# Kernel tuning notes

Measured on AMD Instinct MI355X. Metric: run time of the kernel, lower is better.

Reference implementation:

```python
import jax, jax.numpy as jnp
import numpy as np

B, T, C, H = 16, 512, 256, 8
HS_T = C // H   # temporal head size = 32
HS_S = T // H   # spatial head size = 64
EPS = 1e-6


def _ln(x, w, b):
    m = x.mean(-1, keepdims=True)
    v = ((x - m) ** 2).mean(-1, keepdims=True)
    return (x - m) / jnp.sqrt(v + EPS) * w + b


def setup_inputs() -> dict:
    key = jax.random.key(0)
    ks = jax.random.split(key, 16)
    rn = lambda k, s, scale: jax.random.normal(k, s, dtype=jnp.float32) * scale
    inp = {
        "x_T": rn(ks[0], (B, T, C), 1.0),
        "x_S": rn(ks[1], (B, C, T), 1.0),
        # temporal attention: per-head q/k/v projections, stacked [H, hs, C]
        "Wq_t": rn(ks[2], (H, HS_T, C), C ** -0.5),
        "Wk_t": rn(ks[3], (H, HS_T, C), C ** -0.5),
        "Wv_t": rn(ks[4], (H, HS_T, C), C ** -0.5),
        "Wo": rn(ks[5], (C, C), C ** -0.5),
        # spatial attention: per-head q/k over the time axis, stacked [H, hs_s, T]
        "Wq_s": rn(ks[6], (H, HS_S, T), T ** -0.5),
        "Wk_s": rn(ks[7], (H, HS_S, T), T ** -0.5),
        # feed-forward blocks (expansion_factor=4)
        "ff1_w1": rn(ks[8], (4 * C, C), C ** -0.5),
        "ff1_b1": jnp.zeros((4 * C,), jnp.float32),
        "ff1_w2": rn(ks[9], (C, 4 * C), (4 * C) ** -0.5),
        "ff1_b2": jnp.zeros((C,), jnp.float32),
        "ff2_w1": rn(ks[10], (4 * C, C), C ** -0.5),
        "ff2_b1": jnp.zeros((4 * C,), jnp.float32),
        "ff2_w2": rn(ks[11], (C, 4 * C), (4 * C) ** -0.5),
        "ff2_b2": jnp.zeros((C,), jnp.float32),
        # layernorm affine params
        "t_ln1_w": jnp.ones((C,), jnp.float32), "t_ln1_b": jnp.zeros((C,), jnp.float32),
        "t_ln2_w": jnp.ones((C,), jnp.float32), "t_ln2_b": jnp.zeros((C,), jnp.float32),
        "s_ln1_w": jnp.ones((T,), jnp.float32), "s_ln1_b": jnp.zeros((T,), jnp.float32),
        "fus_ln_w": jnp.ones((C,), jnp.float32), "fus_ln_b": jnp.zeros((C,), jnp.float32),
    }
    return inp


def reference(x_T, x_S, Wq_t, Wk_t, Wv_t, Wo, Wq_s, Wk_s,
              ff1_w1, ff1_b1, ff1_w2, ff1_b2, ff2_w1, ff2_b1, ff2_w2, ff2_b2,
              t_ln1_w, t_ln1_b, t_ln2_w, t_ln2_b, s_ln1_w, s_ln1_b,
              fus_ln_w, fus_ln_b):
    # ---- temporal (causal) multi-head attention ----
    h = _ln(x_T, t_ln1_w, t_ln1_b)                         # [B,T,C]
    q = jnp.einsum('btc,hdc->bhtd', h, Wq_t)
    k = jnp.einsum('btc,hdc->bhtd', h, Wk_t)
    v = jnp.einsum('btc,hdc->bhtd', h, Wv_t)
    scores = jnp.einsum('bhtd,bhsd->bhts', q, k) / jnp.sqrt(jnp.float32(HS_T))
    causal = jnp.tril(jnp.ones((T, T), dtype=bool))
    scores = jnp.where(causal, scores, -jnp.inf)
    att = jax.nn.softmax(scores, axis=-1)
    o = jnp.einsum('bhts,bhsd->bhtd', att, v)              # [B,H,T,hs]
    o = o.transpose(0, 2, 1, 3).reshape(B, T, C)           # concat heads
    attn_out = o @ Wo.T
    x = x_T + attn_out
    # FFN 1
    h2 = _ln(x, t_ln2_w, t_ln2_b)
    f = jax.nn.relu(h2 @ ff1_w1.T + ff1_b1) @ ff1_w2.T + ff1_b2
    temporal_out = x + f                                   # [B,T,C]
    # ---- spatial (non-causal) attention over neurons ----
    hs = _ln(x_S, s_ln1_w, s_ln1_b)                        # [B,C,T]
    qs = jnp.einsum('bct,hdt->bhcd', hs, Wq_s)
    ks = jnp.einsum('bct,hdt->bhcd', hs, Wk_s)
    sc = jnp.einsum('bhcd,bhed->bhce', qs, ks) / jnp.sqrt(jnp.float32(HS_S))
    spatial_weights = jax.nn.softmax(sc, axis=-1).mean(axis=1)   # [B,C,C], mean over heads
    # ---- fusion ----
    fused = jnp.einsum('bce,bte->btc', spatial_weights, temporal_out)
    x2 = temporal_out + fused
    h3 = _ln(x2, fus_ln_w, fus_ln_b)
    f2 = jax.nn.relu(h3 @ ff2_w1.T + ff2_b1) @ ff2_w2.T + ff2_b2
    out = x2 + f2
    return out, spatial_weights
```

## Files before the change

kernel.cpp:

```cpp
#include <hip/hip_runtime.h>
#include <hip/hip_bf16.h>

typedef __hip_bfloat16 bf16;
typedef __attribute__((ext_vector_type(8))) short short8;
typedef __attribute__((ext_vector_type(4))) float f32x4;

#define F_BIAS 1
#define F_RELU 2
#define F_RES  4

__device__ __forceinline__ void st_out(float* p, float v){ *p = v; }
__device__ __forceinline__ void st_out(bf16* p, float v){ *p = __float2bfloat16(v); }
__device__ __forceinline__ short f2bs(float f){
  bf16 h = __float2bfloat16(f);
  return *reinterpret_cast<short*>(&h);
}

__device__ __forceinline__ void gl_lds16(const void* g, void* l){
  __builtin_amdgcn_global_load_lds(
      (const __attribute__((address_space(1))) void*)g,
      (__attribute__((address_space(3))) void*)l, 16, 0, 0);
}

__device__ __forceinline__ void lgkm_barrier(){
  asm volatile("s_waitcnt lgkmcnt(0)" ::: "memory");
  __builtin_amdgcn_s_barrier();
}

struct ProArgs {
  const float* wsrc[10];
  bf16* wdst[10];
  const float *xT, *xS, *tl1w, *tl1b, *sl1w, *sl1b;
  bf16 *hT, *hS;
};

template<int RL>
__device__ __forceinline__ void wave_ln(bf16* __restrict__ dst,
    const float* __restrict__ src, const float* __restrict__ w,
    const float* __restrict__ bvec, int row){
  int lane = threadIdx.x & 63;
  const float* s = src + (size_t)row*RL;
  float4 v0 = *(const float4*)(s + lane*4);
  float4 v1 = {0.f,0.f,0.f,0.f};
  float sum = v0.x+v0.y+v0.z+v0.w;
  float sq  = v0.x*v0.x+v0.y*v0.y+v0.z*v0.z+v0.w*v0.w;
  if (RL == 512){
    v1 = *(const float4*)(s + 256 + lane*4);
    sum += v1.x+v1.y+v1.z+v1.w;
    sq  += v1.x*v1.x+v1.y*v1.y+v1.z*v1.z+v1.w*v1.w;
  }
  #pragma unroll
  for (int off=32; off; off>>=1){
    sum += __shfl_xor(sum, off, 64);
    sq  += __shfl_xor(sq , off, 64);
  }
  const float inv = 1.0f/(float)RL;
  float mean = sum*inv;
  float rstd = rsqrtf(sq*inv - mean*mean + 1e-6f);
  float4 w0 = *(const float4*)(w + lane*4);
  float4 b0 = *(const float4*)(bvec + lane*4);
  bf16* d = dst + (size_t)row*RL;
  short4 o;
  o.x = f2bs((v0.x-mean)*rstd*w0.x + b0.x);
  o.y = f2bs((v0.y-mean)*rstd*w0.y + b0.y);
  o.z = f2bs((v0.z-mean)*rstd*w0.z + b0.z);
  o.w = f2bs((v0.w-mean)*rstd*w0.w + b0.w);
  *(short4*)((short*)d + lane*4) = o;
  if (RL == 512){
    float4 w1 = *(const float4*)(w + 256 + lane*4);
    float4 b1 = *(const float4*)(bvec + 256 + lane*4);
    short4 o1;
    o1.x = f2bs((v1.x-mean)*rstd*w1.x + b1.x);
    o1.y = f2bs((v1.y-mean)*rstd*w1.y + b1.y);
    o1.z = f2bs((v1.z-mean)*rstd*w1.z + b1.z);
    o1.w = f2bs((v1.w-mean)*rstd*w1.w + b1.w);
    *(short4*)((short*)d + 256 + lane*4) = o1;
  }
}

__global__ __launch_bounds__(256) void prologue(ProArgs a){
  int blk = blockIdx.x;
  int wid = threadIdx.x >> 6;
  if (blk < 1792){
    int v = blk*256 + threadIdx.x;
    int e = v*4;
    int seg = (e>=65536)+(e>=131072)+(e>=196608)+(e>=262144)+(e>=524288)
            + (e>=786432)+(e>=1048576)+(e>=1310720)+(e>=1572864);
    const int starts[10] = {0,65536,131072,196608,262144,524288,786432,
                            1048576,1310720,1572864};
    int off = e - starts[seg];
    float4 f = *(const float4*)(a.wsrc[seg] + off);
    short4 o;
    o.x = f2bs(f.x); o.y = f2bs(f.y); o.z = f2bs(f.z); o.w = f2bs(f.w);
    *(short4*)((short*)a.wdst[seg] + off) = o;
  } else if (blk < 1792 + 2048){
    wave_ln<256>(a.hT, a.xT, a.tl1w, a.tl1b, (blk-1792)*4 + wid);
  } else {
    wave_ln<512>(a.hS, a.xS, a.sl1w, a.sl1b, (blk-3840)*4 + wid);
  }
}

template<int BM, int BN, int BK>
__device__ __forceinline__ void gemm_body(
    short* __restrict__ AsB, short* __restrict__ BsB,
    const bf16* __restrict__ A, const bf16* __restrict__ B,
    float* __restrict__ outF, bf16* __restrict__ outB,
    const float* __restrict__ bias, const float* __restrict__ resid,
    int K, int lda, int ldb, int ldc, int flags, int m0, int n0){
  int tid = threadIdx.x;
  int w = tid>>6, lane = tid&63, quad = lane>>4, l16 = lane&15;
  constexpr int MF  = BM/32;
  constexpr int NF  = BN/32;
  constexpr int CPR = BK/8;
  constexpr int CA  = BM*CPR/256;
  constexpr int CB  = BN*CPR/256;
  int wm = (w>>1)*(BM/2), wn = (w&1)*(BN/2);
  f32x4 acc[MF][NF];
  #pragma unroll
  for (int r=0;r<MF;r++)
    #pragma unroll
    for (int j=0;j<NF;j++)
      acc[r][j] = (f32x4){0.f,0.f,0.f,0.f};

  auto stage = [&](int k0, int half){
    short* as = AsB + half*(BM*BK);
    short* bs = BsB + half*(BN*BK);
    #pragma unroll
    for (int c=0;c<CA;c++){
      int ch = tid + c*256;
      int row = ch / CPR, p = ch % CPR;
      gl_lds16(A + (size_t)(m0+row)*lda + k0 + ((p ^ (row&(CPR-1)))*8),
               &as[row*BK + p*8]);
    }
    #pragma unroll
    for (int c=0;c<CB;c++){
      int ch = tid + c*256;
      int row = ch / CPR, p = ch % CPR;
      gl_lds16(B + (size_t)(n0+row)*ldb + k0 + ((p ^ (row&(CPR-1)))*8),
               &bs[row*BK + p*8]);
    }
  };

  stage(0, 0);
  int nk = K / BK;
  for (int t = 0; t < nk; ++t){
    __syncthreads();
    if (t+1 < nk) stage((t+1)*BK, (t+1)&1);
    const short* as = AsB + (t&1)*(BM*BK);
    const short* bs = BsB + (t&1)*(BN*BK);
    #pragma unroll
    for (int ks=0; ks<BK/32; ++ks){
      short8 af[MF], bfr[NF];
      #pragma unroll
      for (int r=0;r<MF;r++){
        int rr = wm + r*16 + l16;
        af[r] = *(short8*)&as[rr*BK + (((ks*4+quad) ^ (rr&(CPR-1)))*8)];
      }
      #pragma unroll
      for (int j=0;j<NF;j++){
        int rr = wn + j*16 + l16;
        bfr[j] = *(short8*)&bs[rr*BK + (((ks*4+quad) ^ (rr&(CPR-1)))*8)];
      }
      #pragma unroll
      for (int r=0;r<MF;r++)
        #pragma unroll
        for (int j=0;j<NF;j++)
          acc[r][j] = __builtin_amdgcn_mfma_f32_16x16x32_bf16(af[r], bfr[j], acc[r][j], 0,0,0);
    }
  }
  #pragma unroll
  for (int r=0;r<MF;r++){
    int mb = m0 + wm + r*16 + quad*4;
    #pragma unroll
    for (int j=0;j<NF;j++){
      int n = n0 + wn + j*16 + l16;
      float bv = (flags & F_BIAS) ? bias[n] : 0.0f;
      #pragma unroll
      for (int e=0;e<4;e++){
        float v = acc[r][j][e] + bv;
        if (flags & F_RELU) v = fmaxf(v, 0.0f);
        long long idx = (long long)(mb+e)*ldc + n;
        if (flags & F_RES) v += resid[idx];
        if (outF) outF[idx] = v;
        if (outB) st_out(outB + idx, v);
      }
    }
  }
}

struct GArgs {
  const bf16 *A, *B;
  float* outF; bf16* outB;
  const float *bias, *resid;
  int K, lda, ldb, ldc, flags, ty;
};
__global__ __launch_bounds__(256) void gemm_dual(GArgs g0, GArgs g1, int n0){
  __shared__ __align__(16) short As[2*64*64];
  __shared__ __align__(16) short Bs[2*128*64];
  int id = blockIdx.x;
  bool first = id < n0;
  const GArgs& g = first ? g0 : g1;
  int t = first ? id : id - n0;
  int bx = t / g.ty, by = t - bx*g.ty;
  gemm_body<64,128,64>(As, Bs, g.A, g.B, g.outF, g.outB, g.bias, g.resid,
                       g.K, g.lda, g.ldb, g.ldc, g.flags, bx*64, by*128);
}

__global__ __launch_bounds__(512) void gemm_ln(
    const bf16* __restrict__ A, const bf16* __restrict__ B,
    float* __restrict__ outF, bf16* __restrict__ outLN,
    const float* __restrict__ resid,
    const float* __restrict__ lnw, const float* __restrict__ lnb,
    int K, int lda, int ldb, int flags,
    long long sA, long long sB, long long sO, long long sR){
  int bz = blockIdx.z;
  A += (size_t)bz*sA;
  B += (size_t)bz*sB;
  long long obase = (long long)bz*sO;
  __shared__ __align__(16) short As[2*32*64];
  __shared__ __align__(16) short Bs[2*256*64];
  __shared__ float redS[4][32], redQ[4][32];
  int tid = threadIdx.x;
  int m0 = blockIdx.x*32;
  int w = tid>>6, lane = tid&63, quad = lane>>4, l16 = lane&15;
  int wm = (w>>2)*16;
  int wn = (w&3)*64;
  f32x4 acc[4];
  #pragma unroll
  for (int j=0;j<4;j++) acc[j] = (f32x4){0.f,0.f,0.f,0.f};

  auto stage = [&](int k0, int half){
    short* as = As + half*(32*64);
    short* bs = Bs + half*(256*64);
    if (tid < 256){
      int row = tid >> 3, p = tid & 7;
      gl_lds16(A + (size_t)(m0+row)*lda + k0 + ((p ^ (row&7))*8),
               &as[row*64 + p*8]);
    }
    #pragma unroll
    for (int c=0;c<4;c++){
      int ch = tid + c*512;
      int row = ch >> 3, p = ch & 7;
      gl_lds16(B + (size_t)row*ldb + k0 + ((p ^ (row&7))*8),
               &bs[row*64 + p*8]);
    }
  };

  stage(0, 0);
  int nk = K / 64;
  for (int t = 0; t < nk; ++t){
    __syncthreads();
    if (t+1 < nk) stage((t+1)*64, (t+1)&1);
    const short* as = As + (t&1)*(32*64);
    const short* bs = Bs + (t&1)*(256*64);
    #pragma unroll
    for (int ks=0; ks<2; ++ks){
      int rr = wm + l16;
      short8 af = *(short8*)&as[rr*64 + (((ks*4+quad) ^ (rr&7))*8)];
      #pragma unroll
      for (int j=0;j<4;j++){
        int rb = wn + j*16 + l16;
        short8 bfr = *(short8*)&bs[rb*64 + (((ks*4+quad) ^ (rb&7))*8)];
        acc[j] = __builtin_amdgcn_mfma_f32_16x16x32_bf16(af, bfr, acc[j], 0,0,0);
      }
    }
  }
  #pragma unroll
  for (int e=0;e<4;e++){
    int row = wm + quad*4 + e;
    float s = 0.f, q2 = 0.f;
    #pragma unroll
    for (int j=0;j<4;j++){
      float v = acc[j][e];
      if (flags & F_RES)
        v += resid[(long long)bz*sR + (long long)(m0+row)*256 + wn + j*16 + l16];
      acc[j][e] = v;
      s += v; q2 += v*v;
    }
    #pragma unroll
    for (int off=1; off<16; off<<=1){
      s  += __shfl_xor(s , off, 16);
      q2 += __shfl_xor(q2, off, 16);
    }
    if (l16==0){ redS[w&3][row] = s; redQ[w&3][row] = q2; }
  }
  __syncthreads();
  #pragma unroll
  for (int e=0;e<4;e++){
    int row = wm + quad*4 + e;
    float tot = redS[0][row] + redS[1][row] + redS[2][row] + redS[3][row];
    float tq  = redQ[0][row] + redQ[1][row] + redQ[2][row] + redQ[3][row];
    float mean = tot * (1.0f/256.0f);
    float var  = tq * (1.0f/256.0f) - mean*mean;
    float rstd = rsqrtf(var + 1e-6f);
    #pragma unroll
    for (int j=0;j<4;j++){
      int col = wn + j*16 + l16;
      float v = acc[j][e];
      long long idx = obase + (long long)(m0+row)*256 + col;
      if (outF) outF[idx] = v;
      outLN[idx] = __float2bfloat16((v-mean)*rstd*lnw[col] + lnb[col]);
    }
  }
}

struct FfnArgs {
  const bf16 *A;
  const bf16 *W1;
  const float *B1;
  const bf16 *W2;
  const float *B2;
  const float *resid;
  float *outF;
  bf16  *outB;
};

__global__ __launch_bounds__(512) void ffn(FfnArgs a){
  __shared__ __align__(16) short Afull[32*256];
  __shared__ __align__(16) short Hs[32*1024];
  __shared__ __align__(16) short Bst[2*16384];
  int tid = threadIdx.x;
  int w = tid>>6, lane = tid&63, quad = lane>>4, l16 = lane&15;
  int m0 = blockIdx.x*32;
  int wm  = (w>>2)*16;
  int wnA = (w&3)*32;
  int wnB = (w&3)*64;

  #pragma unroll
  for (int c=0;c<2;c++){
    int ch = tid + c*512;
    int row = ch>>5, p = ch&31;
    gl_lds16(a.A + (size_t)(m0+row)*256 + ((p ^ row)*8), &Afull[ch*8]);
  }
  auto stageA = [&](int i, int half){
    short* bs = Bst + half*16384;
    int nc = i>>2, kt = i&3;
    #pragma unroll
    for (int c=0;c<2;c++){
      int ch = tid + c*512;
      int row = ch>>3, p = ch&7;
      gl_lds16(a.W1 + (size_t)(nc*128+row)*256 + kt*64 + ((p ^ (row&7))*8),
               &bs[ch*8]);
    }
  };
  auto stageB = [&](int kt, int half){
    short* bs = Bst + half*16384;
    #pragma unroll
    for (int c=0;c<4;c++){
      int ch = tid + c*512;
      int row = ch>>3, p = ch&7;
      gl_lds16(a.W2 + (size_t)row*1024 + kt*64 + ((p ^ (row&7))*8),
               &bs[ch*8]);
    }
  };

  stageA(0, 0);
  f32x4 acc[2];
  for (int i=0; i<32; ++i){
    __syncthreads();
    if (i+1 < 32) stageA(i+1, (i+1)&1);
    const short* bs = Bst + (i&1)*16384;
    int kt = i&3, nc = i>>2;
    if (kt==0){
      acc[0] = (f32x4){0.f,0.f,0.f,0.f};
      acc[1] = (f32x4){0.f,0.f,0.f,0.f};
    }
    #pragma unroll
    for (int ks=0; ks<2; ++ks){
      int rr = wm + l16;
      int kk = kt*8 + ks*4 + quad;
      short8 af = *(short8*)&Afull[rr*256 + ((kk ^ rr)*8)];
      #pragma unroll
      for (int j=0;j<2;j++){
        int rb = wnA + j*16 + l16;
        short8 bk = *(short8*)&bs[rb*64 + (((ks*4+quad) ^ (rb&7))*8)];
        acc[j] = __builtin_amdgcn_mfma_f32_16x16x32_bf16(af, bk, acc[j], 0,0,0);
      }
    }
    if (kt==3){
      #pragma unroll
      for (int j=0;j<2;j++)
        #pragma unroll
        for (int e=0;e<4;e++){
          int row = wm + quad*4 + e;
          int col = nc*128 + wnA + j*16 + l16;
          float v = fmaxf(acc[j][e] + a.B1[col], 0.0f);
          int grp = col>>3;
          Hs[row*1024 + ((grp ^ (row&7))<<3) + (col&7)] = f2bs(v);
        }
    }
  }

  stageB(0, 0);
  __syncthreads();
  f32x4 accB[4];
  #pragma unroll
  for (int j=0;j<4;j++) accB[j] = (f32x4){0.f,0.f,0.f,0.f};
  for (int kt=0; kt<16; ++kt){
    if (kt) __syncthreads();
    if (kt+1 < 16) stageB(kt+1, (kt+1)&1);
    const short* bs = Bst + (kt&1)*16384;
    #pragma unroll
    for (int ks=0; ks<2; ++ks){
      int rr = wm + l16;
      int kk = kt*8 + ks*4 + quad;
      short8 af = *(short8*)&Hs[rr*1024 + ((kk ^ (rr&7))*8)];
      #pragma unroll
      for (int j=0;j<4;j++){
        int rb = wnB + j*16 + l16;
        short8 bk = *(short8*)&bs[rb*64 + (((ks*4+quad) ^ (rb&7))*8)];
        accB[j] = __builtin_amdgcn_mfma_f32_16x16x32_bf16(af, bk, accB[j], 0,0,0);
      }
    }
  }
  #pragma unroll
  for (int j=0;j<4;j++){
    int n = wnB + j*16 + l16;
    float bv = a.B2[n];
    #pragma unroll
    for (int e=0;e<4;e++){
      int row = m0 + wm + quad*4 + e;
      long long idx = (long long)row*256 + n;
      float v = accB[j][e] + bv + a.resid[idx];
      a.outF[idx] = v;
      if (a.outB) st_out(a.outB + idx, v);
    }
  }
}

__device__ __forceinline__ int fsw(int row){ return (row>>1)&3; }
__global__ __launch_bounds__(256) void flash_mfma(
    const bf16* __restrict__ qkv, bf16* __restrict__ o){
  int qt = (int)gridDim.x - 1 - (int)blockIdx.x;
  int h = blockIdx.y, b = blockIdx.z;
  int tid = threadIdx.x;
  int w = tid>>6, lane = tid&63, quad = lane>>4, l16 = lane&15;
  __shared__ __align__(16) bf16 Qs[64*32];
  __shared__ __align__(16) bf16 Ks[2][64*32];
  __shared__ __align__(16) bf16 Vt[2][32*72];
  __shared__ __align__(16) bf16 Ps[64*72];
  const bf16* base = qkv + (size_t)b*512*768;
  int t0 = qt*64;
  int srow = tid>>2, spos = tid&3;
  gl_lds16(base + (size_t)(t0+srow)*768 + h*32 + ((spos ^ fsw(srow))*8),
           &Qs[srow*32 + spos*8]);
  {
    const bf16* rp = base + (size_t)srow*768 + h*32;
    gl_lds16(rp + 256 + ((spos ^ fsw(srow))*8), &Ks[0][srow*32 + spos*8]);
    short8 v = *(const short8*)(rp + 512 + spos*8);
    #pragma unroll
    for (int q=0;q<8;q++){
      short tmp = v[q];
      Vt[0][(spos*8+q)*72 + srow] = *(bf16*)&tmp;
    }
  }
  f32x4 accO[2];
  accO[0] = (f32x4){0.f,0.f,0.f,0.f};
  accO[1] = (f32x4){0.f,0.f,0.f,0.f};
  float m_i[4], l_i[4];
  #pragma unroll
  for (int e=0;e<4;e++){ m_i[e] = -3.0e38f; l_i[e] = 0.0f; }
  const float scale = 0.17677669529663687f;
  __syncthreads();
  int rq = w*16 + l16;
  short8 aq = *(short8*)&Qs[rq*32 + ((quad ^ fsw(rq))*8)];

  for (int kt = 0; kt <= qt; ++kt){
    if (kt) __syncthreads();
    int cur = kt&1, nxt = cur^1;
    bool pre = (kt < qt);
    short8 vpre;
    if (pre){
      const bf16* rp = base + (size_t)((kt+1)*64 + srow)*768 + h*32;
      gl_lds16(rp + 256 + ((spos ^ fsw(srow))*8), &Ks[nxt][srow*32 + spos*8]);
      vpre = *(const short8*)(rp + 512 + spos*8);
    }
    f32x4 S[4];
    #pragma unroll
    for (int j2=0;j2<4;j2++){
      int rk = j2*16 + l16;
      short8 bk = *(short8*)&Ks[cur][rk*32 + ((quad ^ fsw(rk))*8)];
      S[j2] = __builtin_amdgcn_mfma_f32_16x16x32_bf16(aq, bk,
                (f32x4){0.f,0.f,0.f,0.f}, 0,0,0);
    }
    bool diag = (kt == qt);
    int s0 = kt*64;
    int qrow_base = t0 + w*16 + quad*4;
    #pragma unroll
    for (int e=0;e<4;e++){
      float sv[4];
      #pragma unroll
      for (int j2=0;j2<4;j2++){
        float x = S[j2][e]*scale;
        if (diag && (s0 + j2*16 + l16 > qrow_base + e)) x = -3.0e38f;
        sv[j2] = x;
      }
      float mx = fmaxf(fmaxf(sv[0],sv[1]), fmaxf(sv[2],sv[3]));
      #pragma unroll
      for (int off=1; off<16; off<<=1) mx = fmaxf(mx, __shfl_xor(mx, off, 64));
      float m_new = fmaxf(m_i[e], mx);
      float alpha = __expf(m_i[e]-m_new);
      float rs = 0.0f;
      #pragma unroll
      for (int j2=0;j2<4;j2++){
        float p = __expf(sv[j2]-m_new);
        rs += p;
        Ps[(w*16+quad*4+e)*72 + j2*16 + l16] = __float2bfloat16(p);
      }
      #pragma unroll
      for (int off=1; off<16; off<<=1) rs += __shfl_xor(rs, off, 64);
      l_i[e] = l_i[e]*alpha + rs;
      m_i[e] = m_new;
      accO[0][e] *= alpha;
      accO[1][e] *= alpha;
    }
    asm volatile("s_waitcnt lgkmcnt(0)" ::: "memory");
    __builtin_amdgcn_sched_barrier(0);
    #pragma unroll
    for (int sh=0; sh<2; ++sh){
      short8 ap = *(short8*)&Ps[(w*16+l16)*72 + sh*32 + quad*8];
      #pragma unroll
      for (int dh=0; dh<2; ++dh){
        short8 bv = *(short8*)&Vt[cur][(dh*16+l16)*72 + sh*32 + quad*8];
        accO[dh] = __builtin_amdgcn_mfma_f32_16x16x32_bf16(ap, bv, accO[dh], 0,0,0);
      }
    }
    if (pre){
      #pragma unroll
      for (int q=0;q<8;q++){
        short tmp = vpre[q];
        Vt[nxt][(spos*8+q)*72 + srow] = *(bf16*)&tmp;
      }
    }
  }
  #pragma unroll
  for (int e=0;e<4;e++){
    float inv = 1.0f/l_i[e];
    int t = t0 + w*16 + quad*4 + e;
    bf16* op = o + ((size_t)(b*512+t))*256 + h*32 + l16;
    op[0]  = __float2bfloat16(accO[0][e]*inv);
    op[16] = __float2bfloat16(accO[1][e]*inv);
  }
}

__global__ __launch_bounds__(256) void spatial_fused(
    const bf16* __restrict__ qk, float* __restrict__ out1,
    bf16* __restrict__ swB){
  int ct = blockIdx.x & 15, b = blockIdx.x >> 4;
  int tid = threadIdx.x;
  int w = tid>>6, lane = tid&63, quad = lane>>4, l16 = lane&15;
  __shared__ __align__(16) bf16 Qall[16*512];
  __shared__ __align__(16) bf16 Ks[2][256*64];
  __shared__ float redM[4][16], redS2[4][16];
  const bf16* qbase = qk + ((size_t)(b*256 + ct*16))*1024;
  #pragma unroll
  for (int c=0;c<4;c++){
    int ch = tid + c*256;
    int row = ch>>6, p = ch&63;
    gl_lds16(qbase + (size_t)row*1024 + ((p ^ (row&7))*8), &Qall[row*512 + p*8]);
  }
  auto stageK = [&](int h, int half){
    bf16* ks = Ks[half];
    #pragma unroll
    for (int c=0;c<8;c++){
      int ch = tid + c*256;
      int e = ch>>3, p = ch&7;
      gl_lds16(qk + ((size_t)(b*256 + e))*1024 + 512 + h*64 + ((p ^ (e&7))*8),
               &ks[e*64 + p*8]);
    }
  };
  stageK(0, 0);
  float fRes[4][4];
  #pragma unroll
  for (int j=0;j<4;j++)
    #pragma unroll
    for (int e=0;e<4;e++) fRes[j][e] = 0.0f;

  for (int h=0; h<8; ++h){
    __syncthreads();
    if (h+1 < 8) stageK(h+1, (h+1)&1);
    const bf16* kcur = Ks[h&1];
    f32x4 acc[4];
    #pragma unroll
    for (int j=0;j<4;j++) acc[j] = (f32x4){0.f,0.f,0.f,0.f};
    #pragma unroll
    for (int ki=0; ki<2; ++ki){
      int g = h*8 + ki*4 + quad;
      short8 aq = *(short8*)&Qall[l16*512 + ((g ^ (l16&7))*8)];
      #pragma unroll
      for (int j=0;j<4;j++){
        int e = w*64 + j*16 + l16;
        short8 bk = *(short8*)&kcur[e*64 + (((ki*4+quad) ^ (e&7))*8)];
        acc[j] = __builtin_amdgcn_mfma_f32_16x16x32_bf16(aq, bk, acc[j], 0,0,0);
      }
    }
    #pragma unroll
    for (int e=0;e<4;e++){
      float m = -3.0e38f;
      #pragma unroll
      for (int j=0;j<4;j++){
        float s = acc[j][e]*0.125f;
        acc[j][e] = s;
        m = fmaxf(m, s);
      }
      #pragma unroll
      for (int off=1; off<16; off<<=1) m = fmaxf(m, __shfl_xor(m, off, 16));
      if (l16==0) redM[w][quad*4+e] = m;
    }
    lgkm_barrier();
    #pragma unroll
    for (int e=0;e<4;e++){
      int r = quad*4+e;
      float m = fmaxf(fmaxf(redM[0][r],redM[1][r]), fmaxf(redM[2][r],redM[3][r]));
      float s = 0.0f;
      #pragma unroll
      for (int j=0;j<4;j++){
        float p = __expf(acc[j][e]-m);
        acc[j][e] = p; s += p;
      }
      #pragma unroll
      for (int off=1; off<16; off<<=1) s += __shfl_xor(s, off, 16);
      if (l16==0) redS2[w][r] = s;
    }
    lgkm_barrier();
    #pragma unroll
    for (int e=0;e<4;e++){
      int r = quad*4+e;
      float tot = redS2[0][r]+redS2[1][r]+redS2[2][r]+redS2[3][r];
      float inv = 0.125f/tot;
      #pragma unroll
      for (int j=0;j<4;j++) fRes[j][e] += acc[j][e]*inv;
    }
  }
  #pragma unroll
  for (int e=0;e<4;e++){
    int c = ct*16 + quad*4 + e;
    size_t rb = ((size_t)b*256 + c)*256;
    #pragma unroll
    for (int j=0;j<4;j++){
      int col = w*64 + j*16 + l16;
      out1[rb+col] = fRes[j][e];
      swB[rb+col]  = __float2bfloat16(fRes[j][e]);
    }
  }
}

extern "C" void kernel_launch(void* const* d_in, const int* in_sizes, int n_in,
                              void* d_out, int out_size, void* d_ws, size_t ws_size,
                              hipStream_t stream){
  (void)in_sizes; (void)n_in; (void)out_size; (void)ws_size;
  const float* x_T  = (const float*)d_in[0];
  const float* x_S  = (const float*)d_in[1];
  const float* Wq_t = (const float*)d_in[2];
  const float* Wk_t = (const float*)d_in[3];
  const float* Wv_t = (const float*)d_in[4];
  const float* Wo   = (const float*)d_in[5];
  const float* Wq_s = (const float*)d_in[6];
  const float* Wk_s = (const float*)d_in[7];
  const float* f1w1 = (const float*)d_in[8];
  const float* f1b1 = (const float*)d_in[9];
  const float* f1w2 = (const float*)d_in[10];
  const float* f1b2 = (const float*)d_in[11];
  const float* f2w1 = (const float*)d_in[12];
  const float* f2b1 = (const float*)d_in[13];
  const float* f2w2 = (const float*)d_in[14];
  const float* f2b2 = (const float*)d_in[15];
  const float* tl1w = (const float*)d_in[16];
  const float* tl1b = (const float*)d_in[17];
  const float* tl2w = (const float*)d_in[18];
  const float* tl2b = (const float*)d_in[19];
  const float* sl1w = (const float*)d_in[20];
  const float* sl1b = (const float*)d_in[21];
  const float* flw  = (const float*)d_in[22];
  const float* flb  = (const float*)d_in[23];

  float* ws = (float*)d_ws;
  size_t off = 0;
  bf16*  Wqkvb  = (bf16*)(ws + off); off += 768*256/2;
  bf16*  Wob    = (bf16*)(ws + off); off += 256*256/2;
  bf16*  f1w1b  = (bf16*)(ws + off); off += 1024*256/2;
  bf16*  f1w2b  = (bf16*)(ws + off); off += 256*1024/2;
  bf16*  f2w1b  = (bf16*)(ws + off); off += 1024*256/2;
  bf16*  f2w2b  = (bf16*)(ws + off); off += 256*1024/2;
  bf16*  WSb    = (bf16*)(ws + off); off += 1024*512/2;
  bf16*  bufHb  = (bf16*)(ws + off); off += (size_t)8192*256/2;
  bf16*  bufHSb = (bf16*)(ws + off); off += (size_t)4096*512/2;
  bf16*  bufQKVb= (bf16*)(ws + off); off += (size_t)8192*768/2;
  bf16*  bufOb  = (bf16*)(ws + off); off += (size_t)8192*256/2;
  bf16*  bufTOb = (bf16*)(ws + off); off += (size_t)8192*256/2;
  bf16*  swB    = (bf16*)(ws + off); off += (size_t)16*256*256/2;
  bf16*  qkB    = (bf16*)(ws + off); off += (size_t)4096*1024/2;
  float* bufX   = ws + off; off += (size_t)8192*256;
  float* bufTO  = ws + off; off += (size_t)8192*256;
  float* bufX2  = ws + off; off += (size_t)8192*256;

  float* out0 = (float*)d_out;
  float* out1 = out0 + (size_t)16*512*256;

  ProArgs pa;
  pa.wsrc[0]=Wq_t;  pa.wdst[0]=Wqkvb;
  pa.wsrc[1]=Wk_t;  pa.wdst[1]=Wqkvb+65536;
  pa.wsrc[2]=Wv_t;  pa.wdst[2]=Wqkvb+131072;
  pa.wsrc[3]=Wo;    pa.wdst[3]=Wob;
  pa.wsrc[4]=f1w1;  pa.wdst[4]=f1w1b;
  pa.wsrc[5]=f1w2;  pa.wdst[5]=f1w2b;
  pa.wsrc[6]=f2w1;  pa.wdst[6]=f2w1b;
  pa.wsrc[7]=f2w2;  pa.wdst[7]=f2w2b;
  pa.wsrc[8]=Wq_s;  pa.wdst[8]=WSb;
  pa.wsrc[9]=Wk_s;  pa.wdst[9]=WSb+262144;
  pa.xT=x_T; pa.xS=x_S; pa.tl1w=tl1w; pa.tl1b=tl1b;
  pa.sl1w=sl1w; pa.sl1b=sl1b; pa.hT=bufHb; pa.hS=bufHSb;
  prologue<<<4864,256,0,stream>>>(pa);

  GArgs gq, gs;
  gq.A=bufHb;  gq.B=Wqkvb; gq.outF=nullptr; gq.outB=bufQKVb;
  gq.bias=nullptr; gq.resid=nullptr;
  gq.K=256; gq.lda=256; gq.ldb=256; gq.ldc=768; gq.flags=0; gq.ty=6;
  gs.A=bufHSb; gs.B=WSb;   gs.outF=nullptr; gs.outB=qkB;
  gs.bias=nullptr; gs.resid=nullptr;
  gs.K=512; gs.lda=512; gs.ldb=512; gs.ldc=1024; gs.flags=0; gs.ty=8;
  gemm_dual<<<1280,256,0,stream>>>(gq, gs, 768);

  spatial_fused<<<256,256,0,stream>>>(qkB, out1, swB);

  flash_mfma<<<dim3(8,8,16),256,0,stream>>>(bufQKVb, bufOb);
  gemm_ln<<<dim3(256,1,1),512,0,stream>>>(bufOb, Wob, bufX, bufHb,
        x_T, tl2w, tl2b, 256, 256,256, F_RES, 0,0,0,0);
  FfnArgs fa1;
  fa1.A=bufHb; fa1.W1=f1w1b; fa1.B1=f1b1; fa1.W2=f1w2b; fa1.B2=f1b2;
  fa1.resid=bufX; fa1.outF=bufTO; fa1.outB=bufTOb;
  ffn<<<256,512,0,stream>>>(fa1);
  gemm_ln<<<dim3(16,1,16),512,0,stream>>>(bufTOb, swB, bufX2, bufHb,
        bufTO, flw, flb, 256, 256,256, F_RES,
        131072, 65536, 131072, 131072);
  FfnArgs fa2;
  fa2.A=bufHb; fa2.W1=f2w1b; fa2.B1=f2b1; fa2.W2=f2w2b; fa2.B2=f2b2;
  fa2.resid=bufX2; fa2.outF=out0; fa2.outB=nullptr;
  ffn<<<256,512,0,stream>>>(fa2);
}
```

Measured before the change: 294.2 us.

## Fuse GEMM+LayerNorm into FFN kernel and enlarge dual GEMM tile

Merges the gemm_ln kernel with the following FFN kernel into a single lnffn kernel. The normalized activations stay in shared memory, and the pre-LN residual is kept in registers for the final residual add. This removes two launches and the global round trips of the intermediate fp32 and bf16 buffers. It also raises the QKV/spatial dual GEMM tile from 64x128 to 128x128, halving its grid. The costs are a large shared-memory arena (about 144KB) that limits occupancy, and fewer blocks in the dual GEMM.

Result: faster. 285.6 us (-2.9%).

```diff
diff --git a/kernel.cpp b/kernel.cpp
--- a/kernel.cpp
+++ b/kernel.cpp
@@ -195,62 +195,73 @@
   int K, lda, ldb, ldc, flags, ty;
 };
 __global__ __launch_bounds__(256) void gemm_dual(GArgs g0, GArgs g1, int n0){
-  __shared__ __align__(16) short As[2*64*64];
+  __shared__ __align__(16) short As[2*128*64];
   __shared__ __align__(16) short Bs[2*128*64];
   int id = blockIdx.x;
   bool first = id < n0;
   const GArgs& g = first ? g0 : g1;
   int t = first ? id : id - n0;
   int bx = t / g.ty, by = t - bx*g.ty;
-  gemm_body<64,128,64>(As, Bs, g.A, g.B, g.outF, g.outB, g.bias, g.resid,
-                       g.K, g.lda, g.ldb, g.ldc, g.flags, bx*64, by*128);
-}
-
-__global__ __launch_bounds__(512) void gemm_ln(
-    const bf16* __restrict__ A, const bf16* __restrict__ B,
-    float* __restrict__ outF, bf16* __restrict__ outLN,
-    const float* __restrict__ resid,
-    const float* __restrict__ lnw, const float* __restrict__ lnb,
-    int K, int lda, int ldb, int flags,
-    long long sA, long long sB, long long sO, long long sR){
+  gemm_body<128,128,64>(As, Bs, g.A, g.B, g.outF, g.outB, g.bias, g.resid,
+                        g.K, g.lda, g.ldb, g.ldc, g.flags, bx*128, by*128);
+}
+
+struct LnFfnArgs {
+  const bf16 *A;
+  const bf16 *Bm;
+  const float *resid0;
+  const float *lnw, *lnb;
+  const bf16 *W1; const float *B1;
+  const bf16 *W2; const float *B2;
+  float *outF; bf16 *outB;
+  long long sA, sB, sR, sO;
+};
+
+__global__ __launch_bounds__(512) void lnffn(LnFfnArgs a){
+  __shared__ __align__(16) short arena[73728];
+  __shared__ float redS[4][32], redQ[4][32];
   int bz = blockIdx.z;
-  A += (size_t)bz*sA;
-  B += (size_t)bz*sB;
-  long long obase = (long long)bz*sO;
-  __shared__ __align__(16) short As[2*32*64];
-  __shared__ __align__(16) short Bs[2*256*64];
-  __shared__ float redS[4][32], redQ[4][32];
+  const bf16* A  = a.A  + (size_t)bz*a.sA;
+  const bf16* Bm = a.Bm + (size_t)bz*a.sB;
+  long long rbase = (long long)bz*a.sR;
+  long long obase = (long long)bz*a.sO;
   int tid = threadIdx.x;
+  int w = tid>>6, lane = tid&63, quad = lane>>4, l16 = lane&15;
   int m0 = blockIdx.x*32;
-  int w = tid>>6, lane = tid&63, quad = lane>>4, l16 = lane&15;
   int wm = (w>>2)*16;
   int wn = (w&3)*64;
+
+  short* As  = arena;
+  short* Bs  = arena + 4096;
+  short* Hin = arena;
+  short* Hs  = arena + 8192;
+  short* Bst = arena + 40960;
+
   f32x4 acc[4];
   #pragma unroll
   for (int j=0;j<4;j++) acc[j] = (f32x4){0.f,0.f,0.f,0.f};
 
-  auto stage = [&](int k0, int half){
+  auto stage0 = [&](int k0, int half){
     short* as = As + half*(32*64);
     short* bs = Bs + half*(256*64);
     if (tid < 256){
       int row = tid >> 3, p = tid & 7;
-      gl_lds16(A + (size_t)(m0+row)*lda + k0 + ((p ^ (row&7))*8),
+      gl_lds16(A + (size_t)(m0+row)*256 + k0 + ((p ^ (row&7))*8),
                &as[row*64 + p*8]);
     }
     #pragma unroll
     for (int c=0;c<4;c++){
       int ch = tid + c*512;
       int row = ch >> 3, p = ch & 7;
-      gl_lds16(B + (size_t)row*ldb + k0 + ((p ^ (row&7))*8),
+      gl_lds16(Bm + (size_t)row*256 + k0 + ((p ^ (row&7))*8),
                &bs[row*64 + p*8]);
     }
   };
 
-  stage(0, 0);
-  int nk = K / 64;
-  for (int t = 0; t < nk; ++t){
+  stage0(0, 0);
+  for (int t = 0; t < 4; ++t){
     __syncthreads();
-    if (t+1 < nk) stage((t+1)*64, (t+1)&1);
+    if (t+1 < 4) stage0((t+1)*64, (t+1)&1);
     const short* as = As + (t&1)*(32*64);
     const short* bs = Bs + (t&1)*(256*64);
     #pragma unroll
@@ -271,9 +282,7 @@
     float s = 0.f, q2 = 0.f;
     #pragma unroll
     for (int j=0;j<4;j++){
-      float v = acc[j][e];
-      if (flags & F_RES)
-        v += resid[(long long)bz*sR + (long long)(m0+row)*256 + wn + j*16 + l16];
+      float v = acc[j][e] + a.resid0[rbase + (long long)(m0+row)*256 + wn + j*16 + l16];
       acc[j][e] = v;
       s += v; q2 += v*v;
     }
@@ -296,42 +305,12 @@
     #pragma unroll
     for (int j=0;j<4;j++){
       int col = wn + j*16 + l16;
-      float v = acc[j][e];
-      long long idx = obase + (long long)(m0+row)*256 + col;
-      if (outF) outF[idx] = v;
-      outLN[idx] = __float2bfloat16((v-mean)*rstd*lnw[col] + lnb[col]);
-    }
-  }
-}
-
-struct FfnArgs {
-  const bf16 *A;
-  const bf16 *W1;
-  const float *B1;
-  const bf16 *W2;
-  const float *B2;
-  const float *resid;
-  float *outF;
-  bf16  *outB;
-};
-
-__global__ __launch_bounds__(512) void ffn(FfnArgs a){
-  __shared__ __align__(16) short Afull[32*256];
-  __shared__ __align__(16) short Hs[32*1024];
-  __shared__ __align__(16) short Bst[2*16384];
-  int tid = threadIdx.x;
-  int w = tid>>6, lane = tid&63, quad = lane>>4, l16 = lane&15;
-  int m0 = blockIdx.x*32;
-  int wm  = (w>>2)*16;
-  int wnA = (w&3)*32;
-  int wnB = (w&3)*64;
-
-  #pragma unroll
-  for (int c=0;c<2;c++){
-    int ch = tid + c*512;
-    int row = ch>>5, p = ch&31;
-    gl_lds16(a.A + (size_t)(m0+row)*256 + ((p ^ row)*8), &Afull[ch*8]);
-  }
+      float h = (acc[j][e]-mean)*rstd*a.lnw[col] + a.lnb[col];
+      int g = col >> 3;
+      Hin[row*256 + ((g ^ row)*8) + (col&7)] = f2bs(h);
+    }
+  }
+
   auto stageA = [&](int i, int half){
     short* bs = Bst + half*16384;
     int nc = i>>2, kt = i&3;
@@ -343,38 +322,27 @@
                &bs[ch*8]);
     }
   };
-  auto stageB = [&](int kt, int half){
-    short* bs = Bst + half*16384;
-    #pragma unroll
-    for (int c=0;c<4;c++){
-      int ch = tid + c*512;
-      int row = ch>>3, p = ch&7;
-      gl_lds16(a.W2 + (size_t)row*1024 + kt*64 + ((p ^ (row&7))*8),
-               &bs[ch*8]);
-    }
-  };
-
   stageA(0, 0);
-  f32x4 acc[2];
+  f32x4 a2[2];
   for (int i=0; i<32; ++i){
     __syncthreads();
     if (i+1 < 32) stageA(i+1, (i+1)&1);
     const short* bs = Bst + (i&1)*16384;
     int kt = i&3, nc = i>>2;
     if (kt==0){
-      acc[0] = (f32x4){0.f,0.f,0.f,0.f};
-      acc[1] = (f32x4){0.f,0.f,0.f,0.f};
+      a2[0] = (f32x4){0.f,0.f,0.f,0.f};
+      a2[1] = (f32x4){0.f,0.f,0.f,0.f};
     }
     #pragma unroll
     for (int ks=0; ks<2; ++ks){
       int rr = wm + l16;
       int kk = kt*8 + ks*4 + quad;
-      short8 af = *(short8*)&Afull[rr*256 + ((kk ^ rr)*8)];
+      short8 af = *(short8*)&Hin[rr*256 + ((kk ^ rr)*8)];
       #pragma unroll
       for (int j=0;j<2;j++){
-        int rb = wnA + j*16 + l16;
+        int rb = (w&3)*32 + j*16 + l16;
         short8 bk = *(short8*)&bs[rb*64 + (((ks*4+quad) ^ (rb&7))*8)];
-        acc[j] = __builtin_amdgcn_mfma_f32_16x16x32_bf16(af, bk, acc[j], 0,0,0);
+        a2[j] = __builtin_amdgcn_mfma_f32_16x16x32_bf16(af, bk, a2[j], 0,0,0);
       }
     }
     if (kt==3){
@@ -383,21 +351,30 @@
         #pragma unroll
         for (int e=0;e<4;e++){
           int row = wm + quad*4 + e;
-          int col = nc*128 + wnA + j*16 + l16;
-          float v = fmaxf(acc[j][e] + a.B1[col], 0.0f);
-          int grp = col>>3;
-          Hs[row*1024 + ((grp ^ (row&7))<<3) + (col&7)] = f2bs(v);
+          int col = nc*128 + (w&3)*32 + j*16 + l16;
+          float v = fmaxf(a2[j][e] + a.B1[col], 0.0f);
+          int g = col>>3;
+          Hs[row*1024 + ((g ^ (row&7))*8) + (col&7)] = f2bs(v);
         }
     }
   }
 
+  auto stageB = [&](int kt, int half){
+    short* bs = Bst + half*16384;
+    #pragma unroll
+    for (int c=0;c<4;c++){
+      int ch = tid + c*512;
+      int row = ch>>3, p = ch&7;
+      gl_lds16(a.W2 + (size_t)row*1024 + kt*64 + ((p ^ (row&7))*8),
+               &bs[ch*8]);
+    }
+  };
   stageB(0, 0);
-  __syncthreads();
   f32x4 accB[4];
   #pragma unroll
   for (int j=0;j<4;j++) accB[j] = (f32x4){0.f,0.f,0.f,0.f};
   for (int kt=0; kt<16; ++kt){
-    if (kt) __syncthreads();
+    __syncthreads();
     if (kt+1 < 16) stageB(kt+1, (kt+1)&1);
     const short* bs = Bst + (kt&1)*16384;
     #pragma unroll
@@ -407,7 +384,7 @@
       short8 af = *(short8*)&Hs[rr*1024 + ((kk ^ (rr&7))*8)];
       #pragma unroll
       for (int j=0;j<4;j++){
-        int rb = wnB + j*16 + l16;
+        int rb = wn + j*16 + l16;
         short8 bk = *(short8*)&bs[rb*64 + (((ks*4+quad) ^ (rb&7))*8)];
         accB[j] = __builtin_amdgcn_mfma_f32_16x16x32_bf16(af, bk, accB[j], 0,0,0);
       }
@@ -415,13 +392,13 @@
   }
   #pragma unroll
   for (int j=0;j<4;j++){
-    int n = wnB + j*16 + l16;
+    int n = wn + j*16 + l16;
     float bv = a.B2[n];
     #pragma unroll
     for (int e=0;e<4;e++){
-      int row = m0 + wm + quad*4 + e;
-      long long idx = (long long)row*256 + n;
-      float v = accB[j][e] + bv + a.resid[idx];
+      int row = wm + quad*4 + e;
+      long long idx = obase + (long long)(m0+row)*256 + n;
+      float v = accB[j][e] + bv + acc[j][e];
       a.outF[idx] = v;
       if (a.outB) st_out(a.outB + idx, v);
     }
@@ -690,9 +667,7 @@
   bf16*  bufTOb = (bf16*)(ws + off); off += (size_t)8192*256/2;
   bf16*  swB    = (bf16*)(ws + off); off += (size_t)16*256*256/2;
   bf16*  qkB    = (bf16*)(ws + off); off += (size_t)4096*1024/2;
-  float* bufX   = ws + off; off += (size_t)8192*256;
   float* bufTO  = ws + off; off += (size_t)8192*256;
-  float* bufX2  = ws + off; off += (size_t)8192*256;
 
   float* out0 = (float*)d_out;
   float* out1 = out0 + (size_t)16*512*256;
@@ -719,22 +694,23 @@
   gs.A=bufHSb; gs.B=WSb;   gs.outF=nullptr; gs.outB=qkB;
   gs.bias=nullptr; gs.resid=nullptr;
   gs.K=512; gs.lda=512; gs.ldb=512; gs.ldc=1024; gs.flags=0; gs.ty=8;
-  gemm_dual<<<1280,256,0,stream>>>(gq, gs, 768);
+  gemm_dual<<<640,256,0,stream>>>(gq, gs, 384);
 
   spatial_fused<<<256,256,0,stream>>>(qkB, out1, swB);
 
   flash_mfma<<<dim3(8,8,16),256,0,stream>>>(bufQKVb, bufOb);
-  gemm_ln<<<dim3(256,1,1),512,0,stream>>>(bufOb, Wob, bufX, bufHb,
-        x_T, tl2w, tl2b, 256, 256,256, F_RES, 0,0,0,0);
-  FfnArgs fa1;
-  fa1.A=bufHb; fa1.W1=f1w1b; fa1.B1=f1b1; fa1.W2=f1w2b; fa1.B2=f1b2;
-  fa1.resid=bufX; fa1.outF=bufTO; fa1.outB=bufTOb;
-  ffn<<<256,512,0,stream>>>(fa1);
-  gemm_ln<<<dim3(16,1,16),512,0,stream>>>(bufTOb, swB, bufX2, bufHb,
-        bufTO, flw, flb, 256, 256,256, F_RES,
-        131072, 65536, 131072, 131072);
-  FfnArgs fa2;
-  fa2.A=bufHb; fa2.W1=f2w1b; fa2.B1=f2b1; fa2.W2=f2w2b; fa2.B2=f2b2;
-  fa2.resid=bufX2; fa2.outF=out0; fa2.outB=nullptr;
-  ffn<<<256,512,0,stream>>>(fa2);
-}
+
+  LnFfnArgs la1;
+  la1.A=bufOb; la1.Bm=Wob; la1.resid0=x_T; la1.lnw=tl2w; la1.lnb=tl2b;
+  la1.W1=f1w1b; la1.B1=f1b1; la1.W2=f1w2b; la1.B2=f1b2;
+  la1.outF=bufTO; la1.outB=bufTOb;
+  la1.sA=0; la1.sB=0; la1.sR=0; la1.sO=0;
+  lnffn<<<dim3(256,1,1),512,0,stream>>>(la1);
+
+  LnFfnArgs la2;
+  la2.A=bufTOb; la2.Bm=swB; la2.resid0=bufTO; la2.lnw=flw; la2.lnb=flb;
+  la2.W1=f2w1b; la2.B1=f2b1; la2.W2=f2w2b; la2.B2=f2b2;
+  la2.outF=out0; la2.outB=nullptr;
+  la2.sA=131072; la2.sB=65536; la2.sR=131072; la2.sO=131072;
+  lnffn<<<dim3(16,1,16),512,0,stream>>>(la2);
+}
```
